# Kernel optimization log

Hardware: AMD Instinct MI355X
Metric: run time of the kernel (lower is better)

Reference implementation:

```python
import jax, jax.numpy as jnp
import numpy as np

NPERSEG = 128
HOP = 64  # nperseg - noverlap, noverlap = nperseg//2
NFRAMES = 33
NFREQ = 65

def _hann_periodic(n):
    # scipy get_window('hann', n) -> periodic (sym=False) hann window
    return 0.5 - 0.5 * jnp.cos(2.0 * jnp.pi * jnp.arange(n, dtype=jnp.float32) / n)

def setup_inputs() -> dict:
    key = jax.random.key(0)
    ks = jax.random.split(key, 10)
    B, L, S = 2048, 2048, 8
    H = 1024
    return {
        "x": jax.random.normal(ks[0], (B, L, S), dtype=jnp.float32),
        "sensor_weights": jnp.ones((S,), dtype=jnp.float32),
        "W1": jax.random.normal(ks[1], (H, 2145), dtype=jnp.float32) * 0.02,
        "b1": jnp.zeros((H,), dtype=jnp.float32),
        "W2": jax.random.normal(ks[2], (H // 2, H), dtype=jnp.float32) * 0.02,
        "b2": jnp.zeros((H // 2,), dtype=jnp.float32),
        "W3": jax.random.normal(ks[3], (H // 4, H // 2), dtype=jnp.float32) * 0.02,
        "b3": jnp.zeros((H // 4,), dtype=jnp.float32),
        "W4": jax.random.normal(ks[4], (10, H // 4), dtype=jnp.float32) * 0.02,
        "b4": jnp.zeros((10,), dtype=jnp.float32),
    }

def _stft_mag(x):
    # x: (B, L, S) -> |STFT| per sensor: (B, S, NFREQ, NFRAMES), matching scipy.signal.stft defaults
    xs = jnp.transpose(x, (0, 2, 1))  # (B, S, L)
    # boundary='zeros': pad nperseg//2 zeros each side -> L + 128 = 2176, exact multiple (padded=True adds nothing)
    xp = jnp.pad(xs, ((0, 0), (0, 0), (NPERSEG // 2, NPERSEG // 2)))
    idx = jnp.arange(NFRAMES)[:, None] * HOP + jnp.arange(NPERSEG)[None, :]  # (33, 128)
    frames = xp[:, :, idx]  # (B, S, 33, 128)
    win = _hann_periodic(NPERSEG)
    spec = jnp.fft.rfft(frames * win, axis=-1)  # (B, S, 33, 65)
    mag = jnp.abs(spec) / jnp.sum(win)
    return jnp.transpose(mag, (0, 1, 3, 2))  # (B, S, 65, 33) = (B, S, freq, time)

def reference(x, sensor_weights, W1, b1, W2, b2, W3, b3, W4, b4):
    B = x.shape[0]
    mag = _stft_mag(x)  # (B, S, F, T)
    w = jax.nn.softmax(sensor_weights)  # (S,)
    fused = jnp.einsum('s,bsft->bft', w, mag)  # weighted sensor fusion
    h = fused.reshape(B, -1)  # (B, 2145)
    h = jax.nn.relu(h @ W1.T + b1)
    h = jax.nn.relu(h @ W2.T + b2)
    h = jax.nn.relu(h @ W3.T + b3)
    return h @ W4.T + b4
```

## Files before the change

kernel.cpp:

```cpp
#include <hip/hip_runtime.h>
#include <hip/hip_bf16.h>
#include <math.h>

#define NPERSEG 128
#define HOP     64
#define NFRAMES 33
#define NFREQ   65
#define BATCH   2048
#define LEN     2048
#define NSENS   8
#define FEAT    (NFREQ * NFRAMES)
#define FEATP   2176
#define H1      1024
#define H2      512
#define H3      256
#define NOUT    10

#define XROW    2264
#define CWROW   136
#define NB      160
#define MT_PER_WAVE 3

typedef __attribute__((ext_vector_type(8))) short short8;
typedef __attribute__((ext_vector_type(4))) float float4v;
typedef unsigned short ushort;
typedef unsigned int uint;

__device__ __forceinline__ ushort f2b(float v) {
    __hip_bfloat16 h = __float2bfloat16(v);
    return *reinterpret_cast<ushort*>(&h);
}
__device__ __forceinline__ uint pack2(float a, float b) {
    return (uint)f2b(a) | ((uint)f2b(b) << 16);
}
__device__ __forceinline__ float b2f(ushort u) {
    union { uint i; float f; } c; c.i = ((uint)u) << 16; return c.f;
}
__device__ __forceinline__ float b2fu(uint lo16) {
    union { uint i; float f; } c; c.i = lo16 << 16; return c.f;
}
__device__ __forceinline__ void gl_lds16(const void* g, void* l) {
    __builtin_amdgcn_global_load_lds(
        (const __attribute__((address_space(1))) unsigned int*)g,
        (__attribute__((address_space(3))) unsigned int*)l, 16, 0, 0);
}

__global__ void sf_softmax8(const float* __restrict__ w, float* __restrict__ out) {
    if (threadIdx.x == 0) {
        float m = w[0];
        for (int s = 1; s < NSENS; ++s) m = fmaxf(m, w[s]);
        float e[NSENS];
        float sum = 0.f;
        for (int s = 0; s < NSENS; ++s) { e[s] = expf(w[s] - m); sum += e[s]; }
        float inv = 1.0f / sum;
        for (int s = 0; s < NSENS; ++s) out[s] = e[s] * inv;
    }
}

__global__ void sf_basis(ushort* __restrict__ cwg) {
    int e = blockIdx.x * 256 + threadIdx.x;
    if (e >= NB * CWROW) return;
    int n = e / CWROW, k = e - n * CWROW;
    const float TWO_PI = 6.28318530717958647692f;
    float v = 0.f;
    if (k < NPERSEG) {
        float win = 0.5f - 0.5f * cosf(TWO_PI * (float)k / (float)NPERSEG);
        if (n < NFREQ) {
            int r = (n * k) & (NPERSEG - 1);
            v = win * cosf(TWO_PI * (float)r / (float)NPERSEG) * (1.0f / 64.0f);
        } else if (n >= 80 && n < 80 + NFREQ) {
            int r = ((n - 80) * k) & (NPERSEG - 1);
            v = win * sinf(TWO_PI * (float)r / (float)NPERSEG) * (1.0f / 64.0f);
        }
    }
    cwg[e] = f2b(v);
}

__global__ void sf_cvt_w(const float* __restrict__ src, ushort* __restrict__ dst,
                         int N, int K, int Kp) {
    int e = blockIdx.x * 256 + threadIdx.x;
    if (e >= N * Kp) return;
    int n = e / Kp, k = e - n * Kp;
    dst[e] = f2b(k < K ? src[(long)n * K + k] : 0.f);
}

__global__ __launch_bounds__(512, 4)
void sf_stft_fuse(const float* __restrict__ x,
                  const float* __restrict__ wsoft,
                  const ushort* __restrict__ cwg,
                  ushort* __restrict__ h0) {
    __shared__ __align__(16) ushort xbp[NSENS * XROW];
    __shared__ __align__(16) ushort hstage[FEATP];
    __shared__ float wsens[NSENS];

    const int b    = blockIdx.x;
    const int tid  = threadIdx.x;
    const int lane = tid & 63;
    const int wv   = tid >> 6;

    const float4* xb4 = (const float4*)(x + (size_t)b * (LEN * NSENS));
    uint* xw = (uint*)xbp;
    for (int e = tid; e < 2048; e += 512) {
        int i = e >> 1;
        int h = e & 1;
        float4 v0 = xb4[i * 4 + h];
        float4 v1 = xb4[i * 4 + 2 + h];
        int base = (h * 4) * (XROW / 2) + 32 + i;
        xw[base                 ] = pack2(v0.x, v1.x);
        xw[base +     (XROW / 2)] = pack2(v0.y, v1.y);
        xw[base + 2 * (XROW / 2)] = pack2(v0.z, v1.z);
        xw[base + 3 * (XROW / 2)] = pack2(v0.w, v1.w);
    }
    for (int e = tid; e < NSENS * 32; e += 512)
        xw[(e >> 5) * (XROW / 2) + (e & 31)] = 0;
    for (int e = tid; e < NSENS * 76; e += 512) {
        int s = e / 76;
        xw[s * (XROW / 2) + 1056 + (e - s * 76)] = 0;
    }
    if (tid < FEATP - FEAT) hstage[FEAT + tid] = 0;
    if (tid < NSENS) wsens[tid] = wsoft[tid];
    __syncthreads();

    const int col = lane & 15;
    const int q   = lane >> 4;

    float wqa[4];
    *(float4*)wqa = *(const float4*)&wsens[(q & 1) * 4];

    const ushort* abase[MT_PER_WAVE];
    #pragma unroll
    for (int mb = 0; mb < MT_PER_WAVE; ++mb) {
        int mi = wv * MT_PER_WAVE + mb;
        int m  = mi * 16 + col;
        int ta = m >> 3; if (ta > NFRAMES) ta = NFRAMES;
        int sa = m & 7;
        abase[mb] = &xbp[sa * XROW + ta * HOP + q * 8];
    }

    #pragma unroll 1
    for (int np = 0; np < 5; ++np) {
        float4v accR[MT_PER_WAVE], accI[MT_PER_WAVE];
        #pragma unroll
        for (int mb = 0; mb < MT_PER_WAVE; ++mb) {
            accR[mb] = (float4v){0.f, 0.f, 0.f, 0.f};
            accI[mb] = (float4v){0.f, 0.f, 0.f, 0.f};
        }
        #pragma unroll
        for (int ks = 0; ks < 4; ++ks) {
            short8 bR = *(const short8*)&cwg[(np * 16 + col) * CWROW + ks * 32 + q * 8];
            short8 bI = *(const short8*)&cwg[((np + 5) * 16 + col) * CWROW + ks * 32 + q * 8];
            #pragma unroll
            for (int mb = 0; mb < MT_PER_WAVE; ++mb) {
                short8 af = *(const short8*)(abase[mb] + ks * 32);
                accR[mb] = __builtin_amdgcn_mfma_f32_16x16x32_bf16(af, bR, accR[mb], 0, 0, 0);
                accI[mb] = __builtin_amdgcn_mfma_f32_16x16x32_bf16(af, bI, accI[mb], 0, 0, 0);
            }
        }
        int f = np * 16 + col;
        #pragma unroll
        for (int mb = 0; mb < MT_PER_WAVE; ++mb) {
            float ps = 0.f;
            #pragma unroll
            for (int r = 0; r < 4; ++r) {
                float re = accR[mb][r];
                float im = accI[mb][r];
                ps += wqa[r] * sqrtf(re * re + im * im);
            }
            float tot = ps + __shfl_xor(ps, 16, 64);
            int mi = wv * MT_PER_WAVE + mb;
            int t  = mi * 2 + (q >> 1);
            if (((q & 1) == 0) && t < NFRAMES && f < NFREQ)
                hstage[f * NFRAMES + t] = f2b(tot);
        }
    }
    __syncthreads();

    const uint2* hsw = (const uint2*)hstage;
    uint2* ho = (uint2*)(h0 + (size_t)b * FEATP);
    for (int e = tid; e < FEATP / 4; e += 512)
        ho[e] = hsw[e];
}

template <int BN, int WM, int WN, int RELU>
__global__ __launch_bounds__(256)
void sf_gemm_mfma(const ushort* __restrict__ A, const ushort* __restrict__ W,
                  const float* __restrict__ bias, ushort* __restrict__ C,
                  int M, int N, int K) {
    const int MT = WM / 16, NT = WN / 16;
    const int NWN = BN / WN;
    __shared__ __align__(16) ushort As[128 * 32];
    __shared__ __align__(16) ushort Bs[BN * 32];

    const int tid  = threadIdx.x;
    const int lane = tid & 63;
    const int wv   = tid >> 6;
    const int wvm  = wv / NWN;
    const int wvn  = wv % NWN;
    const int col  = lane & 15;
    const int q    = lane >> 4;

    const int m0 = blockIdx.y * 128;
    const int n0 = blockIdx.x * BN;

    const int srow = lane >> 2;
    const int skch = (lane & 3) ^ ((lane >> 3) & 3);
    const int TC   = (128 + BN) / 16;

    float4v acc[MT][NT];
    #pragma unroll
    for (int mi = 0; mi < MT; ++mi)
        #pragma unroll
        for (int ni = 0; ni < NT; ++ni)
            acc[mi][ni] = (float4v){0.f, 0.f, 0.f, 0.f};

    const int fsw = ((col >> 1) & 3);
    int aoff[MT], boff[NT];
    #pragma unroll
    for (int i = 0; i < MT; ++i)
        aoff[i] = (wvm * WM + i * 16 + col) * 32 + ((q ^ fsw) * 8);
    #pragma unroll
    for (int j = 0; j < NT; ++j)
        boff[j] = (wvn * WN + j * 16 + col) * 32 + ((q ^ fsw) * 8);

    for (int k0 = 0; k0 < K; k0 += 32) {
        #pragma unroll
        for (int c = wv; c < TC; c += 4) {
            if (c < 8)
                gl_lds16(A + (size_t)(m0 + c * 16 + srow) * K + k0 + skch * 8,
                         &As[c * 16 * 32]);
            else
                gl_lds16(W + (size_t)(n0 + (c - 8) * 16 + srow) * K + k0 + skch * 8,
                         &Bs[(c - 8) * 16 * 32]);
        }
        __syncthreads();

        short8 af[MT], bf[NT];
        #pragma unroll
        for (int i = 0; i < MT; ++i) af[i] = *(const short8*)&As[aoff[i]];
        #pragma unroll
        for (int j = 0; j < NT; ++j) bf[j] = *(const short8*)&Bs[boff[j]];
        #pragma unroll
        for (int mi = 0; mi < MT; ++mi)
            #pragma unroll
            for (int ni = 0; ni < NT; ++ni)
                acc[mi][ni] = __builtin_amdgcn_mfma_f32_16x16x32_bf16(af[mi], bf[ni], acc[mi][ni], 0, 0, 0);
        __syncthreads();
    }

    #pragma unroll
    for (int ni = 0; ni < NT; ++ni) {
        int n = n0 + wvn * WN + ni * 16 + col;
        float bn = bias[n];
        #pragma unroll
        for (int mi = 0; mi < MT; ++mi) {
            int mbase = m0 + wvm * WM + mi * 16 + q * 4;
            #pragma unroll
            for (int r = 0; r < 4; ++r) {
                float v = acc[mi][ni][r] + bn;
                if (RELU) v = fmaxf(v, 0.f);
                C[(size_t)(mbase + r) * N + n] = f2b(v);
            }
        }
    }
}

__global__ __launch_bounds__(256)
void sf_final(const ushort* __restrict__ h3, const float* __restrict__ W4,
              const float* __restrict__ b4, float* __restrict__ out) {
    int o = blockIdx.x * 256 + threadIdx.x;
    if (o >= BATCH * NOUT) return;
    int m = o / NOUT, n = o - m * NOUT;
    const uint2*  av = (const uint2*)(h3 + (size_t)m * H3);
    const float4* wv4 = (const float4*)(W4 + (size_t)n * H3);
    float s = 0.f;
    #pragma unroll 8
    for (int j = 0; j < H3 / 4; ++j) {
        uint2 a = av[j];
        float4 w = wv4[j];
        s = fmaf(b2fu(a.x & 0xffffu), w.x, s);
        s = fmaf(b2fu(a.x >> 16),     w.y, s);
        s = fmaf(b2fu(a.y & 0xffffu), w.z, s);
        s = fmaf(b2fu(a.y >> 16),     w.w, s);
    }
    out[o] = s + b4[n];
}

extern "C" void kernel_launch(void* const* d_in, const int* in_sizes, int n_in,
                              void* d_out, int out_size, void* d_ws, size_t ws_size,
                              hipStream_t stream) {
    const float* x  = (const float*)d_in[0];
    const float* sw = (const float*)d_in[1];
    const float* W1 = (const float*)d_in[2];
    const float* b1 = (const float*)d_in[3];
    const float* W2 = (const float*)d_in[4];
    const float* b2 = (const float*)d_in[5];
    const float* W3 = (const float*)d_in[6];
    const float* b3 = (const float*)d_in[7];
    const float* W4 = (const float*)d_in[8];
    const float* b4 = (const float*)d_in[9];
    float* out = (float*)d_out;

    char* cur = (char*)d_ws;
    float* wsoft = (float*)cur;                 cur += 64;
    ushort* cwg  = (ushort*)cur;                cur += NB * CWROW * 2;
    ushort* h0   = (ushort*)cur;                cur += (size_t)BATCH * FEATP * 2;
    ushort* W1b  = (ushort*)cur;                cur += (size_t)H1 * FEATP * 2;
    ushort* W2b  = (ushort*)cur;                cur += (size_t)H2 * H1 * 2;
    ushort* W3b  = (ushort*)cur;                cur += (size_t)H3 * H2 * 2;
    ushort* h1   = (ushort*)cur;                cur += (size_t)BATCH * H1 * 2;
    ushort* h2   = (ushort*)cur;                cur += (size_t)BATCH * H2 * 2;
    ushort* h3   = (ushort*)cur;                cur += (size_t)BATCH * H3 * 2;

    sf_softmax8<<<1, 64, 0, stream>>>(sw, wsoft);
    sf_basis<<<(NB * CWROW + 255) / 256, 256, 0, stream>>>(cwg);
    sf_cvt_w<<<(H1 * FEATP + 255) / 256, 256, 0, stream>>>(W1, W1b, H1, FEAT, FEATP);
    sf_cvt_w<<<(H2 * H1 + 255) / 256, 256, 0, stream>>>(W2, W2b, H2, H1, H1);
    sf_cvt_w<<<(H3 * H2 + 255) / 256, 256, 0, stream>>>(W3, W3b, H3, H2, H2);

    sf_stft_fuse<<<BATCH, 512, 0, stream>>>(x, wsoft, cwg, h0);

    sf_gemm_mfma<64, 32, 64, 1><<<dim3(H1 / 64, BATCH / 128), 256, 0, stream>>>(h0, W1b, b1, h1, BATCH, H1, FEATP);
    sf_gemm_mfma<64, 32, 64, 1><<<dim3(H2 / 64, BATCH / 128), 256, 0, stream>>>(h1, W2b, b2, h2, BATCH, H2, H1);
    sf_gemm_mfma<64, 32, 64, 1><<<dim3(H3 / 64, BATCH / 128), 256, 0, stream>>>(h2, W3b, b3, h3, BATCH, H3, H2);
    sf_final<<<(BATCH * NOUT + 255) / 256, 256, 0, stream>>>(h3, W4, b4, out);
}
```

Measured before the change: 328.8 us.

## Use single-wave double-buffered MFMA GEMMs and merge prep kernels

Replaces the 4-wave 128xBN GEMM with a one-wave kernel. Each wave computes a 64x64 (or 32x64) tile with K steps of 64 and double-buffered global-to-LDS loads, with no block barriers. The softmax, DFT-basis and weight-conversion launches are merged into one prep kernel, and the softmax is computed inline in the STFT kernel. The DFT basis is stored in MFMA fragment order so each lane reads it contiguously. This trims launch overhead and barrier stalls. The trade-off is smaller blocks with less cross-wave reuse, and it relies on implicit wait handling for the LDS DMA loads.

```diff
diff --git a/kernel.cpp b/kernel.cpp
--- a/kernel.cpp
+++ b/kernel.cpp
@@ -17,9 +17,8 @@
 #define NOUT    10
 
 #define XROW    2264
-#define CWROW   136
-#define NB      160
 #define MT_PER_WAVE 3
+#define NCWS    (10 * 4 * 64 * 8)
 
 typedef __attribute__((ext_vector_type(8))) short short8;
 typedef __attribute__((ext_vector_type(4))) float float4v;
@@ -33,9 +32,6 @@
 __device__ __forceinline__ uint pack2(float a, float b) {
     return (uint)f2b(a) | ((uint)f2b(b) << 16);
 }
-__device__ __forceinline__ float b2f(ushort u) {
-    union { uint i; float f; } c; c.i = ((uint)u) << 16; return c.f;
-}
 __device__ __forceinline__ float b2fu(uint lo16) {
     union { uint i; float f; } c; c.i = lo16 << 16; return c.f;
 }
@@ -45,53 +41,48 @@
         (__attribute__((address_space(3))) unsigned int*)l, 16, 0, 0);
 }
 
-__global__ void sf_softmax8(const float* __restrict__ w, float* __restrict__ out) {
-    if (threadIdx.x == 0) {
-        float m = w[0];
-        for (int s = 1; s < NSENS; ++s) m = fmaxf(m, w[s]);
-        float e[NSENS];
-        float sum = 0.f;
-        for (int s = 0; s < NSENS; ++s) { e[s] = expf(w[s] - m); sum += e[s]; }
-        float inv = 1.0f / sum;
-        for (int s = 0; s < NSENS; ++s) out[s] = e[s] * inv;
-    }
-}
-
-__global__ void sf_basis(ushort* __restrict__ cwg) {
+__global__ __launch_bounds__(256)
+void sf_prep(const float* __restrict__ W1, const float* __restrict__ W2,
+             const float* __restrict__ W3,
+             ushort* __restrict__ cws, ushort* __restrict__ W1b,
+             ushort* __restrict__ W2b, ushort* __restrict__ W3b) {
+    const int N1 = NCWS;
+    const int N2 = N1 + H1 * FEATP;
+    const int N3 = N2 + H2 * H1;
+    const int N4 = N3 + H3 * H2;
     int e = blockIdx.x * 256 + threadIdx.x;
-    if (e >= NB * CWROW) return;
-    int n = e / CWROW, k = e - n * CWROW;
-    const float TWO_PI = 6.28318530717958647692f;
-    float v = 0.f;
-    if (k < NPERSEG) {
-        float win = 0.5f - 0.5f * cosf(TWO_PI * (float)k / (float)NPERSEG);
-        if (n < NFREQ) {
-            int r = (n * k) & (NPERSEG - 1);
-            v = win * cosf(TWO_PI * (float)r / (float)NPERSEG) * (1.0f / 64.0f);
-        } else if (n >= 80 && n < 80 + NFREQ) {
-            int r = ((n - 80) * k) & (NPERSEG - 1);
-            v = win * sinf(TWO_PI * (float)r / (float)NPERSEG) * (1.0f / 64.0f);
-        }
-    }
-    cwg[e] = f2b(v);
-}
-
-__global__ void sf_cvt_w(const float* __restrict__ src, ushort* __restrict__ dst,
-                         int N, int K, int Kp) {
-    int e = blockIdx.x * 256 + threadIdx.x;
-    if (e >= N * Kp) return;
-    int n = e / Kp, k = e - n * Kp;
-    dst[e] = f2b(k < K ? src[(long)n * K + k] : 0.f);
+    const float STEP = 6.28318530717958647692f / 128.0f;
+    if (e < N1) {
+        int j = e & 7, l = (e >> 3) & 63, ks = (e >> 9) & 3, tile = e >> 11;
+        int n = tile * 16 + (l & 15);
+        int k = ks * 32 + (l >> 4) * 8 + j;
+        float win = 0.5f - 0.5f * cosf(STEP * (float)k);
+        float v = 0.f;
+        if (n < NFREQ)
+            v = win * cosf(STEP * (float)((n * k) & 127)) * (1.0f / 64.0f);
+        else if (n >= 80 && n < 80 + NFREQ)
+            v = win * sinf(STEP * (float)(((n - 80) * k) & 127)) * (1.0f / 64.0f);
+        cws[e] = f2b(v);
+    } else if (e < N2) {
+        int e2 = e - N1;
+        int n = e2 / FEATP, k = e2 - n * FEATP;
+        W1b[e2] = f2b(k < FEAT ? W1[(long)n * FEAT + k] : 0.f);
+    } else if (e < N3) {
+        int e2 = e - N2;
+        W2b[e2] = f2b(W2[e2]);
+    } else if (e < N4) {
+        int e2 = e - N3;
+        W3b[e2] = f2b(W3[e2]);
+    }
 }
 
 __global__ __launch_bounds__(512, 4)
 void sf_stft_fuse(const float* __restrict__ x,
-                  const float* __restrict__ wsoft,
-                  const ushort* __restrict__ cwg,
+                  const float* __restrict__ sw,
+                  const ushort* __restrict__ cws,
                   ushort* __restrict__ h0) {
     __shared__ __align__(16) ushort xbp[NSENS * XROW];
     __shared__ __align__(16) ushort hstage[FEATP];
-    __shared__ float wsens[NSENS];
 
     const int b    = blockIdx.x;
     const int tid  = threadIdx.x;
@@ -118,14 +109,23 @@
         xw[s * (XROW / 2) + 1056 + (e - s * 76)] = 0;
     }
     if (tid < FEATP - FEAT) hstage[FEAT + tid] = 0;
-    if (tid < NSENS) wsens[tid] = wsoft[tid];
     __syncthreads();
 
     const int col = lane & 15;
     const int q   = lane >> 4;
 
     float wqa[4];
-    *(float4*)wqa = *(const float4*)&wsens[(q & 1) * 4];
+    {
+        float s0 = sw[0], s1 = sw[1], s2 = sw[2], s3 = sw[3];
+        float s4 = sw[4], s5 = sw[5], s6 = sw[6], s7 = sw[7];
+        float mx = fmaxf(fmaxf(fmaxf(s0, s1), fmaxf(s2, s3)),
+                         fmaxf(fmaxf(s4, s5), fmaxf(s6, s7)));
+        float e0 = expf(s0 - mx), e1 = expf(s1 - mx), e2 = expf(s2 - mx), e3 = expf(s3 - mx);
+        float e4 = expf(s4 - mx), e5 = expf(s5 - mx), e6 = expf(s6 - mx), e7 = expf(s7 - mx);
+        float inv = 1.0f / (e0 + e1 + e2 + e3 + e4 + e5 + e6 + e7);
+        if ((q & 1) == 0) { wqa[0] = e0 * inv; wqa[1] = e1 * inv; wqa[2] = e2 * inv; wqa[3] = e3 * inv; }
+        else              { wqa[0] = e4 * inv; wqa[1] = e5 * inv; wqa[2] = e6 * inv; wqa[3] = e7 * inv; }
+    }
 
     const ushort* abase[MT_PER_WAVE];
     #pragma unroll
@@ -137,6 +137,7 @@
         abase[mb] = &xbp[sa * XROW + ta * HOP + q * 8];
     }
 
+    ushort* h0b = h0 + (size_t)b * FEATP;
     #pragma unroll 1
     for (int np = 0; np < 5; ++np) {
         float4v accR[MT_PER_WAVE], accI[MT_PER_WAVE];
@@ -147,8 +148,8 @@
         }
         #pragma unroll
         for (int ks = 0; ks < 4; ++ks) {
-            short8 bR = *(const short8*)&cwg[(np * 16 + col) * CWROW + ks * 32 + q * 8];
-            short8 bI = *(const short8*)&cwg[((np + 5) * 16 + col) * CWROW + ks * 32 + q * 8];
+            short8 bR = *(const short8*)&cws[(((np * 4) + ks) * 64 + lane) * 8];
+            short8 bI = *(const short8*)&cws[((((np + 5) * 4) + ks) * 64 + lane) * 8];
             #pragma unroll
             for (int mb = 0; mb < MT_PER_WAVE; ++mb) {
                 short8 af = *(const short8*)(abase[mb] + ks * 32);
@@ -176,84 +177,86 @@
     __syncthreads();
 
     const uint2* hsw = (const uint2*)hstage;
-    uint2* ho = (uint2*)(h0 + (size_t)b * FEATP);
+    uint2* ho = (uint2*)(h0b);
     for (int e = tid; e < FEATP / 4; e += 512)
         ho[e] = hsw[e];
 }
 
-template <int BN, int WM, int WN, int RELU>
-__global__ __launch_bounds__(256)
-void sf_gemm_mfma(const ushort* __restrict__ A, const ushort* __restrict__ W,
-                  const float* __restrict__ bias, ushort* __restrict__ C,
-                  int M, int N, int K) {
-    const int MT = WM / 16, NT = WN / 16;
-    const int NWN = BN / WN;
-    __shared__ __align__(16) ushort As[128 * 32];
-    __shared__ __align__(16) ushort Bs[BN * 32];
-
-    const int tid  = threadIdx.x;
-    const int lane = tid & 63;
-    const int wv   = tid >> 6;
-    const int wvm  = wv / NWN;
-    const int wvn  = wv % NWN;
+template <int MT, int RELU>
+__global__ __launch_bounds__(64)
+void sf_gemm1w(const ushort* __restrict__ A, const ushort* __restrict__ W,
+               const float* __restrict__ bias, ushort* __restrict__ C,
+               int M, int N, int K) {
+    const int BM = MT * 16;
+    __shared__ __align__(16) ushort As[2][BM * 64];
+    __shared__ __align__(16) ushort Bs[2][64 * 64];
+
+    const int lane = threadIdx.x;
     const int col  = lane & 15;
     const int q    = lane >> 4;
-
-    const int m0 = blockIdx.y * 128;
-    const int n0 = blockIdx.x * BN;
-
-    const int srow = lane >> 2;
-    const int skch = (lane & 3) ^ ((lane >> 3) & 3);
-    const int TC   = (128 + BN) / 16;
-
-    float4v acc[MT][NT];
+    const int m0 = blockIdx.y * BM;
+    const int n0 = blockIdx.x * 64;
+
+    const int srow = lane >> 3;
+    const int skch = (lane & 7) ^ srow;
+
+    const ushort* ag = A + (size_t)(m0 + srow) * K + skch * 8;
+    const ushort* wg = W + (size_t)(n0 + srow) * K + skch * 8;
+
+    float4v acc[MT][4];
     #pragma unroll
     for (int mi = 0; mi < MT; ++mi)
         #pragma unroll
-        for (int ni = 0; ni < NT; ++ni)
+        for (int ni = 0; ni < 4; ++ni)
             acc[mi][ni] = (float4v){0.f, 0.f, 0.f, 0.f};
 
-    const int fsw = ((col >> 1) & 3);
-    int aoff[MT], boff[NT];
-    #pragma unroll
-    for (int i = 0; i < MT; ++i)
-        aoff[i] = (wvm * WM + i * 16 + col) * 32 + ((q ^ fsw) * 8);
-    #pragma unroll
-    for (int j = 0; j < NT; ++j)
-        boff[j] = (wvn * WN + j * 16 + col) * 32 + ((q ^ fsw) * 8);
-
-    for (int k0 = 0; k0 < K; k0 += 32) {
-        #pragma unroll
-        for (int c = wv; c < TC; c += 4) {
-            if (c < 8)
-                gl_lds16(A + (size_t)(m0 + c * 16 + srow) * K + k0 + skch * 8,
-                         &As[c * 16 * 32]);
-            else
-                gl_lds16(W + (size_t)(n0 + (c - 8) * 16 + srow) * K + k0 + skch * 8,
-                         &Bs[(c - 8) * 16 * 32]);
-        }
-        __syncthreads();
-
-        short8 af[MT], bf[NT];
-        #pragma unroll
-        for (int i = 0; i < MT; ++i) af[i] = *(const short8*)&As[aoff[i]];
-        #pragma unroll
-        for (int j = 0; j < NT; ++j) bf[j] = *(const short8*)&Bs[boff[j]];
-        #pragma unroll
-        for (int mi = 0; mi < MT; ++mi)
-            #pragma unroll
-            for (int ni = 0; ni < NT; ++ni)
-                acc[mi][ni] = __builtin_amdgcn_mfma_f32_16x16x32_bf16(af[mi], bf[ni], acc[mi][ni], 0, 0, 0);
-        __syncthreads();
-    }
-
-    #pragma unroll
-    for (int ni = 0; ni < NT; ++ni) {
-        int n = n0 + wvn * WN + ni * 16 + col;
+    #pragma unroll
+    for (int i = 0; i < MT * 2; ++i)
+        gl_lds16(ag + (size_t)(8 * i) * K, &As[0][i * 512]);
+    #pragma unroll
+    for (int i = 0; i < 8; ++i)
+        gl_lds16(wg + (size_t)(8 * i) * K, &Bs[0][i * 512]);
+
+    const int nk = K >> 6;
+    const int fs = col & 7;
+    for (int kt = 0; kt < nk; ++kt) {
+        const int buf = kt & 1;
+        short8 afr[2][MT], bfr[2][4];
+        #pragma unroll
+        for (int ks = 0; ks < 2; ++ks) {
+            #pragma unroll
+            for (int mi = 0; mi < MT; ++mi)
+                afr[ks][mi] = *(const short8*)&As[buf][(mi * 16 + col) * 64 + (((ks * 4 + q) ^ fs) * 8)];
+            #pragma unroll
+            for (int ni = 0; ni < 4; ++ni)
+                bfr[ks][ni] = *(const short8*)&Bs[buf][(ni * 16 + col) * 64 + (((ks * 4 + q) ^ fs) * 8)];
+        }
+        if (kt + 1 < nk) {
+            const size_t ko = (size_t)(kt + 1) * 64;
+            #pragma unroll
+            for (int i = 0; i < MT * 2; ++i)
+                gl_lds16(ag + (size_t)(8 * i) * K + ko, &As[buf ^ 1][i * 512]);
+            #pragma unroll
+            for (int i = 0; i < 8; ++i)
+                gl_lds16(wg + (size_t)(8 * i) * K + ko, &Bs[buf ^ 1][i * 512]);
+        }
+        #pragma unroll
+        for (int ks = 0; ks < 2; ++ks)
+            #pragma unroll
+            for (int mi = 0; mi < MT; ++mi)
+                #pragma unroll
+                for (int ni = 0; ni < 4; ++ni)
+                    acc[mi][ni] = __builtin_amdgcn_mfma_f32_16x16x32_bf16(
+                        afr[ks][mi], bfr[ks][ni], acc[mi][ni], 0, 0, 0);
+    }
+
+    #pragma unroll
+    for (int ni = 0; ni < 4; ++ni) {
+        int n = n0 + ni * 16 + col;
         float bn = bias[n];
         #pragma unroll
         for (int mi = 0; mi < MT; ++mi) {
-            int mbase = m0 + wvm * WM + mi * 16 + q * 4;
+            int mbase = m0 + mi * 16 + q * 4;
             #pragma unroll
             for (int r = 0; r < 4; ++r) {
                 float v = acc[mi][ni][r] + bn;
@@ -270,7 +273,7 @@
     int o = blockIdx.x * 256 + threadIdx.x;
     if (o >= BATCH * NOUT) return;
     int m = o / NOUT, n = o - m * NOUT;
-    const uint2*  av = (const uint2*)(h3 + (size_t)m * H3);
+    const uint2*  av  = (const uint2*)(h3 + (size_t)m * H3);
     const float4* wv4 = (const float4*)(W4 + (size_t)n * H3);
     float s = 0.f;
     #pragma unroll 8
@@ -301,8 +304,7 @@
     float* out = (float*)d_out;
 
     char* cur = (char*)d_ws;
-    float* wsoft = (float*)cur;                 cur += 64;
-    ushort* cwg  = (ushort*)cur;                cur += NB * CWROW * 2;
+    ushort* cws  = (ushort*)cur;                cur += (size_t)NCWS * 2;
     ushort* h0   = (ushort*)cur;                cur += (size_t)BATCH * FEATP * 2;
     ushort* W1b  = (ushort*)cur;                cur += (size_t)H1 * FEATP * 2;
     ushort* W2b  = (ushort*)cur;                cur += (size_t)H2 * H1 * 2;
@@ -311,16 +313,13 @@
     ushort* h2   = (ushort*)cur;                cur += (size_t)BATCH * H2 * 2;
     ushort* h3   = (ushort*)cur;                cur += (size_t)BATCH * H3 * 2;
 
-    sf_softmax8<<<1, 64, 0, stream>>>(sw, wsoft);
-    sf_basis<<<(NB * CWROW + 255) / 256, 256, 0, stream>>>(cwg);
-    sf_cvt_w<<<(H1 * FEATP + 255) / 256, 256, 0, stream>>>(W1, W1b, H1, FEAT, FEATP);
-    sf_cvt_w<<<(H2 * H1 + 255) / 256, 256, 0, stream>>>(W2, W2b, H2, H1, H1);
-    sf_cvt_w<<<(H3 * H2 + 255) / 256, 256, 0, stream>>>(W3, W3b, H3, H2, H2);
-
-    sf_stft_fuse<<<BATCH, 512, 0, stream>>>(x, wsoft, cwg, h0);
-
-    sf_gemm_mfma<64, 32, 64, 1><<<dim3(H1 / 64, BATCH / 128), 256, 0, stream>>>(h0, W1b, b1, h1, BATCH, H1, FEATP);
-    sf_gemm_mfma<64, 32, 64, 1><<<dim3(H2 / 64, BATCH / 128), 256, 0, stream>>>(h1, W2b, b2, h2, BATCH, H2, H1);
-    sf_gemm_mfma<64, 32, 64, 1><<<dim3(H3 / 64, BATCH / 128), 256, 0, stream>>>(h2, W3b, b3, h3, BATCH, H3, H2);
+    const int n_prep = NCWS + H1 * FEATP + H2 * H1 + H3 * H2;
+    sf_prep<<<(n_prep + 255) / 256, 256, 0, stream>>>(W1, W2, W3, cws, W1b, W2b, W3b);
+
+    sf_stft_fuse<<<BATCH, 512, 0, stream>>>(x, sw, cws, h0);
+
+    sf_gemm1w<4, 1><<<dim3(H1 / 64, BATCH / 64), 64, 0, stream>>>(h0, W1b, b1, h1, BATCH, H1, FEATP);
+    sf_gemm1w<4, 1><<<dim3(H2 / 64, BATCH / 64), 64, 0, stream>>>(h1, W2b, b2, h2, BATCH, H2, H1);
+    sf_gemm1w<2, 1><<<dim3(H3 / 64, BATCH / 32), 64, 0, stream>>>(h2, W3b, b3, h3, BATCH, H3, H2);
     sf_final<<<(BATCH * NOUT + 255) / 256, 256, 0, stream>>>(h3, W4, b4, out);
 }
```

Result: faster. 297.4 us (-9.6%).
